# Performance work log

Measured on AMD Instinct MI355X. Metric: run time of the kernel, lower is better.

## Reference

```python
import jax, jax.numpy as jnp
import numpy as np

INPUT_DIM, ENC_H, DEC_H, HORIZON = 8, 384, 384, 18
B, L = 1024, 336


def _lstm_layer(xs, Wih, Whh, bih, bhh):
    # xs: [B, L, D] -> outputs [B, L, H], final h [B, H]
    Bv = xs.shape[0]
    Hh = Whh.shape[1]
    def step(carry, x_t):
        h, c = carry
        z = x_t @ Wih.T + h @ Whh.T + bih + bhh  # [B, 4H], gate order i,f,g,o (PyTorch)
        i, f, g, o = jnp.split(z, 4, axis=-1)
        c = jax.nn.sigmoid(f) * c + jax.nn.sigmoid(i) * jnp.tanh(g)
        h = jax.nn.sigmoid(o) * jnp.tanh(c)
        return (h, c), h
    init = (jnp.zeros((Bv, Hh), xs.dtype), jnp.zeros((Bv, Hh), xs.dtype))
    (h, c), ys = jax.lax.scan(step, init, jnp.swapaxes(xs, 0, 1))
    return jnp.swapaxes(ys, 0, 1), h


def setup_inputs() -> dict:
    key = jax.random.key(0)
    ks = jax.random.split(key, 20)
    s = 0.05
    d = {
        "x": jax.random.normal(ks[0], (B, L, INPUT_DIM), jnp.float32),
        "future_feats": jax.random.normal(ks[1], (B, HORIZON, 4), jnp.float32),
        # encoder layer 0
        "enc_Wih0": jax.random.normal(ks[2], (4 * ENC_H, INPUT_DIM), jnp.float32) * s,
        "enc_Whh0": jax.random.normal(ks[3], (4 * ENC_H, ENC_H), jnp.float32) * s,
        "enc_bih0": jax.random.normal(ks[4], (4 * ENC_H,), jnp.float32) * s,
        "enc_bhh0": jax.random.normal(ks[5], (4 * ENC_H,), jnp.float32) * s,
        # encoder layer 1
        "enc_Wih1": jax.random.normal(ks[6], (4 * ENC_H, ENC_H), jnp.float32) * s,
        "enc_Whh1": jax.random.normal(ks[7], (4 * ENC_H, ENC_H), jnp.float32) * s,
        "enc_bih1": jax.random.normal(ks[8], (4 * ENC_H,), jnp.float32) * s,
        "enc_bhh1": jax.random.normal(ks[9], (4 * ENC_H,), jnp.float32) * s,
        # attention projection (no bias)
        "Wa": jax.random.normal(ks[10], (DEC_H, ENC_H), jnp.float32) * s,
        # dec_in: Linear(1+4+enc_h -> dec_h)
        "dec_in_W": jax.random.normal(ks[11], (DEC_H, 1 + 4 + ENC_H), jnp.float32) * s,
        "dec_in_b": jax.random.normal(ks[12], (DEC_H,), jnp.float32) * s,
        # decoder LSTM (1 layer)
        "dec_Wih": jax.random.normal(ks[13], (4 * DEC_H, DEC_H), jnp.float32) * s,
        "dec_Whh": jax.random.normal(ks[14], (4 * DEC_H, DEC_H), jnp.float32) * s,
        "dec_bih": jax.random.normal(ks[15], (4 * DEC_H,), jnp.float32) * s,
        "dec_bhh": jax.random.normal(ks[16], (4 * DEC_H,), jnp.float32) * s,
        # output head
        "out_W": jax.random.normal(ks[17], (1, DEC_H), jnp.float32) * s,
        "out_b": jax.random.normal(ks[18], (1,), jnp.float32) * s,
    }
    return d


def reference(x, future_feats, enc_Wih0, enc_Whh0, enc_bih0, enc_bhh0,
              enc_Wih1, enc_Whh1, enc_bih1, enc_bhh1, Wa, dec_in_W, dec_in_b,
              dec_Wih, dec_Whh, dec_bih, dec_bhh, out_W, out_b):
    Bv = x.shape[0]
    # 2-layer encoder (eval mode: inter-layer dropout inactive)
    h1, _ = _lstm_layer(x, enc_Wih0, enc_Whh0, enc_bih0, enc_bhh0)
    enc_out, h_last = _lstm_layer(h1, enc_Wih1, enc_Whh1, enc_bih1, enc_bhh1)
    proj = enc_out @ Wa.T  # [B, L, dec_h] (Wa(enc_out) is step-invariant)

    def dec_step(carry, feat_t):
        h, c, y_prev = carry
        scores = jnp.einsum('bld,bd->bl', proj, h)
        alpha = jax.nn.softmax(scores, axis=1)
        ctx = jnp.einsum('bl,bld->bd', alpha, enc_out)
        din = jnp.concatenate([y_prev, feat_t, ctx], axis=1)  # [B, 1+4+enc_h]
        din = jax.nn.relu(din @ dec_in_W.T + dec_in_b)
        z = din @ dec_Wih.T + h @ dec_Whh.T + dec_bih + dec_bhh
        i, f, g, o = jnp.split(z, 4, axis=-1)
        c = jax.nn.sigmoid(f) * c + jax.nn.sigmoid(i) * jnp.tanh(g)
        h = jax.nn.sigmoid(o) * jnp.tanh(c)
        y_t = h @ out_W.T + out_b  # [B, 1]
        y_prev = jax.lax.stop_gradient(y_t)  # .detach() in torch
        return (h, c, y_prev), y_t

    init = (h_last, jnp.zeros_like(h_last), jnp.zeros((Bv, 1), x.dtype))
    _, ys = jax.lax.scan(dec_step, init, jnp.swapaxes(future_feats, 0, 1))
    return jnp.swapaxes(ys, 0, 1)  # [B, horizon, 1]
```

## Files before the change

### kernel.cpp

```cpp
#include <hip/hip_runtime.h>
#include <stdint.h>

typedef __bf16 bf16;
typedef __bf16 bf16x8 __attribute__((ext_vector_type(8)));
typedef short  s16x8  __attribute__((ext_vector_type(8)));
typedef float  f32x4  __attribute__((ext_vector_type(4)));
typedef uint32_t u32;

#define NB   1024
#define LSEQ 336
#define HID  384
#define HOR  18
#define SMEM_BYTES 36864
#define E1T  ((size_t)24*NB*16)

__device__ bf16  g_H0[(size_t)(LSEQ+1)*NB*HID];
__device__ bf16  g_E1[(size_t)(LSEQ+1)*E1T];
__device__ bf16  g_enc[(size_t)NB*LSEQ*HID];
__device__ bf16  g_Adec[2*NB*768];
__device__ bf16  g_Adin[NB*416];
__device__ bf16  g_xb[NB*LSEQ*8];
__device__ float g_cdec[NB*HID];
__device__ float g_u[NB*HID];
__device__ float g_bias0[1536], g_bias1[1536], g_biasd[1536], g_biasdin[384];
__device__ bf16  g_Bp0[12*13*4096];
__device__ bf16  g_Bp1n[24*24*4*64*8];
__device__ bf16  g_Bpd[12*24*4096];
__device__ bf16  g_Bpi[3*13*4096];
__device__ bf16  g_Bpu[3*12*4096];
__device__ int   g_f0 [8*LSEQ*12*16];
__device__ int   g_f0m[8*LSEQ*12*16];
__device__ int   g_f1 [4*(LSEQ+1)*24*16];

__device__ __forceinline__ float sigf(float x){ return 1.0f/(1.0f + __expf(-x)); }
__device__ __forceinline__ float tanh_f(float x){
  x = fminf(fmaxf(x, -15.f), 15.f);
  float e = __expf(2.f*x);
  return (e - 1.f)/(e + 1.f);
}

__global__ void zero_state_k(){
  int i = blockIdx.x*blockDim.x + threadIdx.x;
  int st = gridDim.x*blockDim.x;
  bf16 z = (bf16)0.f;
  for(int k=i;k<NB*HID;k+=st){ g_H0[k]=z; g_E1[k]=z; g_cdec[k]=0.f; }
  for(int k=i;k<8*LSEQ*12*16;k+=st){ g_f0[k]=0; g_f0m[k]=0; }
  for(int k=i;k<4*(LSEQ+1)*24*16;k+=st) g_f1[k]=0;
}

__global__ void pack_xb_k(const float* __restrict__ x){
  int i = blockIdx.x*256 + threadIdx.x;
  int n = NB*LSEQ*8;
  for(int k=i; k<n; k+=gridDim.x*256) g_xb[k] = (bf16)x[k];
}

__global__ void pack_gates_k(int mode, const float* __restrict__ W1, const float* __restrict__ W2,
                             int nks){
  bf16* out = (mode==0)? g_Bp0 : g_Bpd;
  size_t idx = (size_t)blockIdx.x*256 + threadIdx.x;
  size_t total = (size_t)12*nks*512;
  if(idx >= total) return;
  int lane = (int)(idx & 63);
  int tt   = (int)((idx>>6) & 7);
  size_t tmp = idx >> 9;
  int ks = (int)(tmp % nks);
  int jb = (int)(tmp / nks);
  int n  = (tt>>1)*HID + jb*32 + (tt&1)*16 + (lane&15);
  int kb = ks*32 + (lane>>4)*8;
  bf16x8 v;
  #pragma unroll
  for(int i=0;i<8;i++){
    int k = kb + i;
    float f;
    if(mode==0) f = (k<384) ? W1[(size_t)n*384 + k] : (k<392 ? W2[(size_t)n*8 + (k-384)] : 0.f);
    else        f = (k<384) ? W1[(size_t)n*384 + k] : W2[(size_t)n*384 + (k-384)];
    v[i] = (bf16)f;
  }
  *(bf16x8*)(out + idx*8) = v;
}

__global__ void pack_gates16_k(const float* __restrict__ Wih1, const float* __restrict__ Whh1){
  int idx = blockIdx.x*256 + threadIdx.x;
  if(idx >= 24*24*4*64) return;
  int lane = idx&63, rem = idx>>6;
  int g = rem&3; rem >>= 2;
  int ks = rem%24, jn = rem/24;
  int n  = g*HID + jn*16 + (lane&15);
  int kb = ks*32 + (lane>>4)*8;
  bf16x8 v;
  #pragma unroll
  for(int i=0;i<8;i++){
    int k = kb+i;
    float f = (k<384)? Wih1[(size_t)n*384 + k] : Whh1[(size_t)n*384 + (k-384)];
    v[i] = (bf16)f;
  }
  *(bf16x8*)(g_Bp1n + (size_t)idx*8) = v;
}

__global__ void pack_plain_k(int mode, const float* __restrict__ W, int nks, int nb_cnt){
  bf16* out = mode ? g_Bpu : g_Bpi;
  size_t idx = (size_t)blockIdx.x*256 + threadIdx.x;
  size_t total = (size_t)nb_cnt*nks*512;
  if(idx>=total) return;
  int lane = (int)(idx&63);
  int tt   = (int)((idx>>6)&7);
  size_t tmp = idx>>9;
  int ks = (int)(tmp%nks);
  int nb = (int)(tmp/nks);
  int n  = nb*128 + tt*16 + (lane&15);
  int kb = ks*32 + (lane>>4)*8;
  bf16x8 v;
  #pragma unroll
  for(int i=0;i<8;i++){
    int k = kb+i;
    float f;
    if(mode==0) f = (k<389)? W[(size_t)n*389 + k] : 0.f;
    else        f = W[(size_t)k*384 + n];
    v[i]=(bf16)f;
  }
  *(bf16x8*)(out + idx*8) = v;
}

__global__ void prep_misc_k(const float* bih0,const float* bhh0,const float* bih1,const float* bhh1,
                            const float* dbih,const float* dbhh,const float* dinb){
  int i = blockIdx.x*256 + threadIdx.x;
  if(i<1536){ g_bias0[i]=bih0[i]+bhh0[i]; g_bias1[i]=bih1[i]+bhh1[i]; g_biasd[i]=dbih[i]+dbhh[i]; }
  if(i<384) g_biasdin[i]=dinb[i];
}

__device__ __forceinline__ void spin_set(int* p){
  while(__hip_atomic_load(p, __ATOMIC_RELAXED, __HIP_MEMORY_SCOPE_AGENT) == 0)
    __builtin_amdgcn_s_sleep(2);
}
__device__ __forceinline__ void flag_set(int* p){
  __hip_atomic_store(p, 1, __ATOMIC_RELAXED, __HIP_MEMORY_SCOPE_AGENT);
}
__device__ __forceinline__ void release_agent(){
  __builtin_amdgcn_fence(__ATOMIC_RELEASE, "agent");
}

__global__ __launch_bounds__(256,1)
void enc10_k(){
  extern __shared__ char lds[];
  const int bid = blockIdx.x, tid = threadIdx.x;
  const int lane = tid&63, wv = tid>>6;
  const int l15 = lane&15, lk = (lane>>4)*8;

  if(bid < 96){
    const int g = bid & 7, jb = bid >> 3;
    { const s16x8* src = (const s16x8*)(g_Bp0 + (size_t)jb*13*4096);
      s16x8* dst = (s16x8*)lds;
      #pragma unroll
      for(int h=0;h<26;h++) dst[tid + h*256] = src[tid + h*256];
    }
    bf16* tr = (bf16*)(lds + 13*8192);
    __syncthreads();
    const int jj0 = jb*32 + l15;
    float bia[2],bfa[2],bga[2],boa[2];
    #pragma unroll
    for(int jh=0;jh<2;jh++){
      bia[jh]=g_bias0[jj0+jh*16];     bfa[jh]=g_bias0[384+jj0+jh*16];
      bga[jh]=g_bias0[768+jj0+jh*16]; boa[jh]=g_bias0[1152+jj0+jh*16];
    }
    size_t hoff[2], xoff[2];
    #pragma unroll
    for(int mt=0;mt<2;mt++){
      int row = g*128 + wv*32 + mt*16 + l15;
      hoff[mt] = (size_t)row*HID + lk;
      xoff[mt] = (size_t)row*LSEQ*8;
    }
    float c[2][2][4] = {};
    for(int w=0; w<LSEQ; w++){
      if(w>=1 && tid<12) spin_set(&g_f0[((g*LSEQ + (w-1))*12 + tid)*16]);
      __syncthreads();
      asm volatile("" ::: "memory");
      const bf16* H0w = g_H0 + (size_t)w*NB*HID;
      bf16x8 af[13][2];
      #pragma unroll
      for(int ks=0;ks<12;ks++)
        #pragma unroll
        for(int mt=0;mt<2;mt++)
          af[ks][mt] = *(const bf16x8*)(H0w + hoff[mt] + ks*32);
      #pragma unroll
      for(int mt=0;mt<2;mt++){
        bf16x8 z;
        #pragma unroll
        for(int e=0;e<8;e++) z[e]=(bf16)0.f;
        if(lk==0) z = *(const bf16x8*)(g_xb + xoff[mt] + (size_t)w*8);
        af[12][mt] = z;
      }
      f32x4 acc[2][8];
      #pragma unroll
      for(int m2=0;m2<2;m2++)
        #pragma unroll
        for(int tt=0;tt<8;tt++) acc[m2][tt] = (f32x4){0.f,0.f,0.f,0.f};
      #pragma unroll
      for(int ks=0;ks<13;ks++){
        #pragma unroll
        for(int tt=0;tt<8;tt++){
          bf16x8 bfr = *(const bf16x8*)(lds + (ks*8+tt)*1024 + lane*16);
          acc[0][tt] = __builtin_amdgcn_mfma_f32_16x16x32_bf16(af[ks][0], bfr, acc[0][tt],0,0,0);
          acc[1][tt] = __builtin_amdgcn_mfma_f32_16x16x32_bf16(af[ks][1], bfr, acc[1][tt],0,0,0);
        }
      }
      #pragma unroll
      for(int mt=0;mt<2;mt++)
        #pragma unroll
        for(int jh=0;jh<2;jh++)
          #pragma unroll
          for(int r=0;r<4;r++){
            float zi=acc[mt][0+jh][r]+bia[jh], zf=acc[mt][2+jh][r]+bfa[jh],
                  zg=acc[mt][4+jh][r]+bga[jh], zo=acc[mt][6+jh][r]+boa[jh];
            float cn = sigf(zf)*c[mt][jh][r] + sigf(zi)*tanh_f(zg);
            c[mt][jh][r]=cn;
            int lr = wv*32 + mt*16 + (lane>>4)*4 + r;
            tr[lr*32 + jh*16 + l15] = (bf16)(sigf(zo)*tanh_f(cn));
          }
      __syncthreads();
      bf16* H0n = g_H0 + (size_t)(w+1)*NB*HID;
      #pragma unroll
      for(int h=0;h<2;h++){
        int p = tid + h*256;
        int row = p>>2, cc = p&3;
        s16x8 v = *(const s16x8*)(tr + row*32 + cc*8);
        *(s16x8*)(H0n + (size_t)(g*128+row)*HID + jb*32 + cc*8) = v;
      }
      __syncthreads();
      if(tid==0){
        release_agent();
        flag_set(&g_f0 [((g*LSEQ + w)*12 + jb)*16]);
        flag_set(&g_f0m[((g*LSEQ + w)*12 + jb)*16]);
      }
    }
  } else {
    const int idx = bid-96, m = (idx&7)>>1, jn = (idx>>3) + (idx&1)*12;
    { const s16x8* src = (const s16x8*)(g_Bp1n + (size_t)jn*24*2048);
      s16x8* dst = (s16x8*)lds;
      #pragma unroll
      for(int h=0;h<24;h++) dst[tid + h*256] = src[tid + h*256];
    }
    bf16* tr = (bf16*)(lds + 24*4096);
    __syncthreads();
    const int jj = jn*16 + l15;
    const float bi=g_bias1[jj], bff=g_bias1[384+jj], bg=g_bias1[768+jj], bo=g_bias1[1152+jj];
    int rows[4]; size_t hoff[4], eo[4];
    const int jn_half = (lane>>4)>>1, colin = ((lane>>4)&1)*8;
    #pragma unroll
    for(int mt=0;mt<4;mt++){
      rows[mt] = m*256 + wv*64 + mt*16 + l15;
      hoff[mt] = (size_t)rows[mt]*HID + lk;
      eo[mt]   = (size_t)jn_half*(NB*16) + (size_t)rows[mt]*16 + colin;
    }
    float c[4][4] = {};
    for(int s=1; s<=LSEQ; s++){
      if(tid<24){
        int gg = 2*m + (tid>=12);
        spin_set(&g_f0m[((gg*LSEQ + (s-1))*12 + (tid%12))*16]);
      }
      __syncthreads();
      asm volatile("" ::: "memory");
      const bf16* H0s = g_H0 + (size_t)s*NB*HID;
      const bf16* Es  = g_E1 + (size_t)(s-1)*E1T;
      bf16x8 ap[8][4];
      #pragma unroll
      for(int d=0; d<8; d++)
        #pragma unroll
        for(int mt=0;mt<4;mt++)
          ap[d][mt] = *(const bf16x8*)(H0s + hoff[mt] + d*32);
      if(s>=2 && tid>=32 && tid<56)
        spin_set(&g_f1[((m*(LSEQ+1) + (s-1))*24 + (tid-32))*16]);
      __syncthreads();
      asm volatile("" ::: "memory");
      f32x4 acc[4][4];
      #pragma unroll
      for(int mt=0;mt<4;mt++)
        #pragma unroll
        for(int g4=0;g4<4;g4++) acc[mt][g4] = (f32x4){0.f,0.f,0.f,0.f};
      #pragma unroll
      for(int ks=0;ks<24;ks++){
        bf16x8 bfr[4];
        #pragma unroll
        for(int g4=0;g4<4;g4++) bfr[g4] = *(const bf16x8*)(lds + (ks*4+g4)*1024 + lane*16);
        bf16x8 a[4];
        #pragma unroll
        for(int mt=0;mt<4;mt++) a[mt] = ap[ks&7][mt];
        int kn = ks+8;
        if(kn<24){
          if(kn<12){
            #pragma unroll
            for(int mt=0;mt<4;mt++) ap[ks&7][mt] = *(const bf16x8*)(H0s + hoff[mt] + kn*32);
          } else {
            #pragma unroll
            for(int mt=0;mt<4;mt++) ap[ks&7][mt] = *(const bf16x8*)(Es + (size_t)(kn-12)*32768 + eo[mt]);
          }
        }
        #pragma unroll
        for(int mt=0;mt<4;mt++)
          #pragma unroll
          for(int g4=0;g4<4;g4++)
            acc[mt][g4] = __builtin_amdgcn_mfma_f32_16x16x32_bf16(a[mt], bfr[g4], acc[mt][g4],0,0,0);
      }
      #pragma unroll
      for(int mt=0;mt<4;mt++)
        #pragma unroll
        for(int r=0;r<4;r++){
          float zi=acc[mt][0][r]+bi, zf=acc[mt][1][r]+bff,
                zg=acc[mt][2][r]+bg, zo=acc[mt][3][r]+bo;
          float cn = sigf(zf)*c[mt][r] + sigf(zi)*tanh_f(zg);
          c[mt][r]=cn;
          int lr = wv*64 + mt*16 + (lane>>4)*4 + r;
          tr[lr*16 + l15] = (bf16)(sigf(zo)*tanh_f(cn));
        }
      __syncthreads();
      bf16* E1w = g_E1 + (size_t)s*E1T + (size_t)jn*(NB*16);
      #pragma unroll
      for(int h=0;h<2;h++){
        int p = tid + h*256;
        int row = p>>1, hf2 = p&1;
        s16x8 v = *(const s16x8*)(tr + row*16 + hf2*8);
        *(s16x8*)(E1w + (size_t)(m*256+row)*16 + hf2*8) = v;
      }
      __syncthreads();
      if(tid==0){
        release_agent();
        flag_set(&g_f1[((m*(LSEQ+1) + s)*24 + jn)*16]);
      }
      if((jn&1)==0 && s>=2){
        const int t_out = s-2;
        const bf16* Ep = g_E1 + (size_t)(s-1)*E1T;
        #pragma unroll
        for(int h=0;h<4;h++){
          int cch = tid + h*256;
          int row = cch>>2, seg = cch&3;
          const bf16* srcp = Ep + (size_t)(jn + (seg>>1))*(NB*16) + (size_t)(m*256+row)*16 + (seg&1)*8;
          s16x8 v = *(const s16x8*)srcp;
          *(s16x8*)(g_enc + ((size_t)(m*256+row)*LSEQ + t_out)*HID + jn*16 + seg*8) = v;
        }
      }
    }
    if(tid<24) spin_set(&g_f1[((m*(LSEQ+1) + LSEQ)*24 + tid)*16]);
    __syncthreads();
    asm volatile("" ::: "memory");
    if((jn&1)==0){
      const bf16* Ep = g_E1 + (size_t)LSEQ*E1T;
      #pragma unroll
      for(int h=0;h<4;h++){
        int cch = tid + h*256;
        int row = cch>>2, seg = cch&3;
        const bf16* srcp = Ep + (size_t)(jn + (seg>>1))*(NB*16) + (size_t)(m*256+row)*16 + (seg&1)*8;
        s16x8 v = *(const s16x8*)srcp;
        *(s16x8*)(g_enc + ((size_t)(m*256+row)*LSEQ + (LSEQ-1))*HID + jn*16 + seg*8) = v;
      }
    }
  }
}

struct SReg { s16x8 a0,a1,b0,b1; };

__device__ __forceinline__ void stage_load(const bf16* __restrict__ A, int ldA,
                                           const bf16* __restrict__ Bk, int tid, SReg& sr){
  int c0 = tid, c1 = tid+256;
  sr.a0 = *(const s16x8*)(A + (size_t)(c0>>2)*ldA + (c0&3)*8);
  sr.a1 = *(const s16x8*)(A + (size_t)(c1>>2)*ldA + (c1&3)*8);
  const s16x8* B8 = (const s16x8*)Bk;
  sr.b0 = B8[c0]; sr.b1 = B8[c1];
}

__device__ __forceinline__ void stage_write(char* Ab, char* Bb, int tid, const SReg& sr){
  int c0 = tid, c1 = tid+256;
  *(s16x8*)(Ab + (c0>>2)*80 + (c0&3)*16) = sr.a0;
  *(s16x8*)(Ab + (c1>>2)*80 + (c1&3)*16) = sr.a1;
  *(s16x8*)(Bb + c0*16) = sr.b0;
  *(s16x8*)(Bb + c1*16) = sr.b1;
}

__device__ __forceinline__ void gemm_core(const bf16* __restrict__ A, int ldA,
                                          const bf16* __restrict__ Bp, int nks,
                                          char* smem, f32x4 acc[4][4]){
  const int tid = threadIdx.x;
  const int lane = tid & 63, wv = tid>>6, wm = wv>>1, wn = wv&1;
  char* Ab0 = smem;            char* Ab1 = smem + 10240;
  char* Bb0 = smem + 20480;    char* Bb1 = smem + 28672;
  f32x4 z = {0.f,0.f,0.f,0.f};
  #pragma unroll
  for(int m=0;m<4;m++)
    #pragma unroll
    for(int g=0;g<4;g++) acc[m][g]=z;
  SReg sr;
  stage_load(A, ldA, Bp, tid, sr);
  stage_write(Ab0, Bb0, tid, sr);
  const int aoff = (wm*64 + (lane&15))*80 + (lane>>4)*16;
  const int boff = wn*1024 + lane*16;
  for(int ks=0; ks<nks; ks++){
    char* Ac = (ks&1)? Ab1: Ab0;
    char* Bc = (ks&1)? Bb1: Bb0;
    char* An = (ks&1)? Ab0: Ab1;
    char* Bn = (ks&1)? Bb0: Bb1;
    bool more = (ks+1)<nks;
    if(more) stage_load(A + (ks+1)*32, ldA, Bp + (size_t)(ks+1)*4096, tid, sr);
    __syncthreads();
    bf16x8 af[4], bfr[4];
    #pragma unroll
    for(int mt=0;mt<4;mt++) af[mt] = *(const bf16x8*)(Ac + aoff + mt*16*80);
    #pragma unroll
    for(int g=0;g<4;g++)    bfr[g] = *(const bf16x8*)(Bc + boff + g*2048);
    #pragma unroll
    for(int mt=0;mt<4;mt++)
      #pragma unroll
      for(int g=0;g<4;g++)
        acc[mt][g] = __builtin_amdgcn_mfma_f32_16x16x32_bf16(af[mt], bfr[g], acc[mt][g], 0,0,0);
    if(more) stage_write(An, Bn, tid, sr);
  }
}

__device__ __forceinline__ void lstm_epi(f32x4 acc[4][4], int mbase, int jb,
     const float* __restrict__ bias, float* __restrict__ cst,
     bf16* __restrict__ d0, int ld0, bf16* __restrict__ d1, size_t ld1){
  int lane = threadIdx.x&63, wv = threadIdx.x>>6, wm = wv>>1, wn = wv&1;
  int j = jb*32 + wn*16 + (lane&15);
  float bi = bias[j], bff = bias[384+j], bg = bias[768+j], bo = bias[1152+j];
  #pragma unroll
  for(int mt=0;mt<4;mt++){
    #pragma unroll
    for(int r=0;r<4;r++){
      int brow = mbase + wm*64 + mt*16 + (lane>>4)*4 + r;
      float zi = acc[mt][0][r]+bi, zf = acc[mt][1][r]+bff,
            zg = acc[mt][2][r]+bg, zo = acc[mt][3][r]+bo;
      size_t ci = (size_t)brow*HID + j;
      float cold = cst[ci];
      float cn = sigf(zf)*cold + sigf(zi)*tanh_f(zg);
      cst[ci] = cn;
      bf16 hb = (bf16)(sigf(zo)*tanh_f(cn));
      d0[(size_t)brow*ld0 + j] = hb;
      if(d1) d1[(size_t)brow*ld1 + j] = hb;
    }
  }
}

__global__ __launch_bounds__(256)
void dec_lstm_k(int t){
  __shared__ char smem[SMEM_BYTES];
  int bid = blockIdx.x, mb = bid/12, jb = bid%12;
  int rs = t&1, wsl = rs^1;
  f32x4 acc[4][4];
  gemm_core(g_Adec + (size_t)rs*NB*768 + (size_t)mb*128*768, 768,
            g_Bpd + (size_t)jb*24*4096, 24, smem, acc);
  lstm_epi(acc, mb*128, jb, g_biasd, g_cdec,
           g_Adec + (size_t)wsl*NB*768 + 384, 768, (bf16*)nullptr, 0);
}

__global__ __launch_bounds__(256)
void plain_gemm_k(int t, int mode, const float* __restrict__ outW,
                  const float* __restrict__ outb, float* __restrict__ out,
                  const float* __restrict__ ff){
  __shared__ char smem[SMEM_BYTES];
  int bid = blockIdx.x, mb = bid/3, nb = bid%3;
  int rs = t&1;
  const bf16* A; int ldA, nks; const bf16* Bp;
  if(mode==1){ A = g_Adec + (size_t)rs*NB*768 + 384; ldA=768; Bp = g_Bpu; nks=12; }
  else       { A = g_Adin;                           ldA=416; Bp = g_Bpi; nks=13; }
  f32x4 acc[4][4];
  gemm_core(A + (size_t)mb*128*ldA, ldA, Bp + (size_t)nb*nks*4096, nks, smem, acc);
  int lane = threadIdx.x&63, wv = threadIdx.x>>6, wm = wv>>1, wn = wv&1;
  bf16* dbf = g_Adec + (size_t)rs*NB*768;
  #pragma unroll
  for(int mt=0;mt<4;mt++){
    #pragma unroll
    for(int ti=0;ti<4;ti++){
      int n = nb*128 + (ti*2+wn)*16 + (lane&15);
      #pragma unroll
      for(int r=0;r<4;r++){
        int brow = mb*128 + wm*64 + mt*16 + (lane>>4)*4 + r;
        float v = acc[mt][ti][r];
        if(mode==0){ v += g_biasdin[n]; v = fmaxf(v,0.f); dbf[(size_t)brow*768 + n] = (bf16)v; }
        else g_u[(size_t)brow*384 + n] = v;
      }
    }
  }
  if(mode==1 && t>=1 && nb==0 && threadIdx.x<128){
    int b = mb*128 + threadIdx.x;
    const s16x8* hp = (const s16x8*)(g_Adec + (size_t)rs*NB*768 + (size_t)b*768 + 384);
    float acc2 = 0.f;
    #pragma unroll 4
    for(int i=0;i<48;i++){
      s16x8 v = hp[i];
      #pragma unroll
      for(int e=0;e<8;e++){
        float hv = __uint_as_float(((u32)(uint16_t)v[e])<<16);
        acc2 += hv*outW[i*8+e];
      }
    }
    float y = acc2 + outb[0];
    out[(size_t)b*HOR + (t-1)] = y;
    g_Adin[(size_t)b*416] = (bf16)y;
    #pragma unroll
    for(int k=0;k<4;k++) g_Adin[(size_t)b*416 + 1 + k] = (bf16)ff[(size_t)b*HOR*4 + t*4 + k];
  }
}

__global__ __launch_bounds__(256)
void attn_k(int t){
  __shared__ float sm[4][392];
  int tid = threadIdx.x, lane = tid&63, w = tid>>6;
  int bl = w>>1, hf = w&1;
  int b = blockIdx.x*2 + bl;
  const float* ub = g_u + (size_t)b*HID + lane*6;
  float u0=ub[0],u1=ub[1],u2=ub[2],u3=ub[3],u4=ub[4],u5=ub[5];
  const u32* er = (const u32*)(g_enc + (size_t)b*LSEQ*HID) + (size_t)hf*168*192 + lane*3;
  int estep = 192;
  if(t & 1){ er += (size_t)167*192; estep = -192; }
  float m=-1e30f, den=0.f, a0=0,a1=0,a2=0,a3=0,a4=0,a5=0;
  for(int l=0;l<168;l++){
    u32 w0 = er[0], w1 = er[1], w2 = er[2];
    er += estep;
    float e0 = __uint_as_float(w0<<16);
    float e1 = __uint_as_float(w0 & 0xffff0000u);
    float e2 = __uint_as_float(w1<<16);
    float e3 = __uint_as_float(w1 & 0xffff0000u);
    float e4 = __uint_as_float(w2<<16);
    float e5 = __uint_as_float(w2 & 0xffff0000u);
    float p = e0*u0 + e1*u1 + e2*u2 + e3*u3 + e4*u4 + e5*u5;
    #pragma unroll
    for(int o=1;o<64;o<<=1) p += __shfl_xor(p, o, 64);
    float mn = fmaxf(m, p);
    float al = __expf(m - mn), pe = __expf(p - mn);
    den = den*al + pe;
    a0 = a0*al + pe*e0; a1 = a1*al + pe*e1; a2 = a2*al + pe*e2;
    a3 = a3*al + pe*e3; a4 = a4*al + pe*e4; a5 = a5*al + pe*e5;
    m = mn;
  }
  if(lane==0){ sm[w][0]=m; sm[w][1]=den; }
  sm[w][2+lane*6+0]=a0; sm[w][2+lane*6+1]=a1; sm[w][2+lane*6+2]=a2;
  sm[w][2+lane*6+3]=a3; sm[w][2+lane*6+4]=a4; sm[w][2+lane*6+5]=a5;
  __syncthreads();
  if(hf==0){
    float m2 = sm[w+1][0], d2 = sm[w+1][1];
    float M = fmaxf(m, m2);
    float f1 = __expf(m - M), f2 = __expf(m2 - M);
    float inv = 1.f/(den*f1 + d2*f2);
    bf16* cd = g_Adin + (size_t)b*416 + 5 + lane*6;
    cd[0] = (bf16)((a0*f1 + sm[w+1][2+lane*6+0]*f2)*inv);
    cd[1] = (bf16)((a1*f1 + sm[w+1][2+lane*6+1]*f2)*inv);
    cd[2] = (bf16)((a2*f1 + sm[w+1][2+lane*6+2]*f2)*inv);
    cd[3] = (bf16)((a3*f1 + sm[w+1][2+lane*6+3]*f2)*inv);
    cd[4] = (bf16)((a4*f1 + sm[w+1][2+lane*6+4]*f2)*inv);
    cd[5] = (bf16)((a5*f1 + sm[w+1][2+lane*6+5]*f2)*inv);
  }
}

__global__ void post_k(int t, const float* __restrict__ outW,
                       const float* __restrict__ outb, float* __restrict__ out){
  int b = blockIdx.x*256 + threadIdx.x;
  if(b>=NB) return;
  int wsl = (t&1)^1;
  const s16x8* hp = (const s16x8*)(g_Adec + (size_t)wsl*NB*768 + (size_t)b*768 + 384);
  float acc = 0.f;
  #pragma unroll 4
  for(int i=0;i<48;i++){
    s16x8 v = hp[i];
    #pragma unroll
    for(int e=0;e<8;e++){
      float hv = __uint_as_float(((u32)(uint16_t)v[e])<<16);
      acc += hv*outW[i*8+e];
    }
  }
  out[(size_t)b*HOR + t] = acc + outb[0];
}

__global__ void dec_prep_k(const float* __restrict__ ff){
  int i = blockIdx.x*256 + threadIdx.x;
  if(i < NB*HID){
    int b = i/HID, j = i%HID;
    g_Adec[(size_t)b*768 + 384 + j] = g_enc[(size_t)b*LSEQ*HID + (size_t)(LSEQ-1)*HID + j];
  }
  if(i < NB*4){
    int b = i>>2, k = i&3;
    g_Adin[(size_t)b*416 + 1 + k] = (bf16)ff[(size_t)b*HOR*4 + k];
  }
  if(i < NB) g_Adin[(size_t)i*416] = (bf16)0.f;
}

extern "C" void kernel_launch(void* const* d_in, const int* in_sizes, int n_in,
                              void* d_out, int out_size, void* d_ws, size_t ws_size,
                              hipStream_t stream){
  const float* x    = (const float*)d_in[0];
  const float* ff   = (const float*)d_in[1];
  const float* Wih0 = (const float*)d_in[2];
  const float* Whh0 = (const float*)d_in[3];
  const float* bih0 = (const float*)d_in[4];
  const float* bhh0 = (const float*)d_in[5];
  const float* Wih1 = (const float*)d_in[6];
  const float* Whh1 = (const float*)d_in[7];
  const float* bih1 = (const float*)d_in[8];
  const float* bhh1 = (const float*)d_in[9];
  const float* Wa   = (const float*)d_in[10];
  const float* dinW = (const float*)d_in[11];
  const float* dinb = (const float*)d_in[12];
  const float* dWih = (const float*)d_in[13];
  const float* dWhh = (const float*)d_in[14];
  const float* dbih = (const float*)d_in[15];
  const float* dbhh = (const float*)d_in[16];
  const float* outW = (const float*)d_in[17];
  const float* outb = (const float*)d_in[18];
  float* out = (float*)d_out;

  zero_state_k<<<1024,256,0,stream>>>();
  pack_xb_k<<<2048,256,0,stream>>>(x);
  pack_gates_k<<<(12*13*512)/256,256,0,stream>>>(0, Whh0, Wih0, 13);
  pack_gates16_k<<<576,256,0,stream>>>(Wih1, Whh1);
  pack_gates_k<<<(12*24*512)/256,256,0,stream>>>(2, dWih, dWhh, 24);
  pack_plain_k<<<(3*13*512)/256,256,0,stream>>>(0, dinW, 13, 3);
  pack_plain_k<<<(3*12*512)/256,256,0,stream>>>(1, Wa, 12, 3);
  prep_misc_k<<<8,256,0,stream>>>(bih0,bhh0,bih1,bhh1,dbih,dbhh,dinb);

  hipFuncSetAttribute((const void*)enc10_k,
                      hipFuncAttributeMaxDynamicSharedMemorySize, 114688);
  enc10_k<<<192,256,114688,stream>>>();

  dec_prep_k<<<1536,256,0,stream>>>(ff);
  for(int t=0;t<HOR;t++){
    plain_gemm_k<<<24,256,0,stream>>>(t, 1, outW, outb, out, ff);
    attn_k<<<512,256,0,stream>>>(t);
    plain_gemm_k<<<24,256,0,stream>>>(t, 0, outW, outb, out, ff);
    dec_lstm_k<<<96,256,0,stream>>>(t);
  }
  post_k<<<4,256,0,stream>>>(17, outW, outb, out);
  (void)in_sizes; (void)n_in; (void)out_size; (void)d_ws; (void)ws_size;
}
```

Measured before the change: 7.595 ms.

## Fuse attention query projection and output head into attention kernel

Removes the per-step MFMA GEMM that computed u = h·Wa into a global buffer. Each attention block now computes its two rows of u itself from a bf16 copy of Wa using scalar FMAs in LDS, and the y_t output dot product moves into otherwise idle threads of the same block. This drops one kernel launch per decoder step and the global round trip of u. The cost is that Wa is read redundantly by all 512 blocks and the projection runs on plain FMAs instead of matrix cores. Encoder output stores also become nontemporal, and the unused second destination is dropped from the LSTM epilogue.

```diff
diff --git a/kernel.cpp b/kernel.cpp
--- a/kernel.cpp
+++ b/kernel.cpp
@@ -20,14 +20,13 @@
 __device__ bf16  g_Adec[2*NB*768];
 __device__ bf16  g_Adin[NB*416];
 __device__ bf16  g_xb[NB*LSEQ*8];
+__device__ bf16  g_Wab[HID*HID];
 __device__ float g_cdec[NB*HID];
-__device__ float g_u[NB*HID];
 __device__ float g_bias0[1536], g_bias1[1536], g_biasd[1536], g_biasdin[384];
 __device__ bf16  g_Bp0[12*13*4096];
 __device__ bf16  g_Bp1n[24*24*4*64*8];
 __device__ bf16  g_Bpd[12*24*4096];
 __device__ bf16  g_Bpi[3*13*4096];
-__device__ bf16  g_Bpu[3*12*4096];
 __device__ int   g_f0 [8*LSEQ*12*16];
 __device__ int   g_f0m[8*LSEQ*12*16];
 __device__ int   g_f1 [4*(LSEQ+1)*24*16];
@@ -48,10 +47,11 @@
   for(int k=i;k<4*(LSEQ+1)*24*16;k+=st) g_f1[k]=0;
 }
 
-__global__ void pack_xb_k(const float* __restrict__ x){
+__global__ void pack_xb_k(const float* __restrict__ x, const float* __restrict__ Wa){
   int i = blockIdx.x*256 + threadIdx.x;
   int n = NB*LSEQ*8;
   for(int k=i; k<n; k+=gridDim.x*256) g_xb[k] = (bf16)x[k];
+  for(int k=i; k<HID*HID; k+=gridDim.x*256) g_Wab[k] = (bf16)Wa[k];
 }
 
 __global__ void pack_gates_k(int mode, const float* __restrict__ W1, const float* __restrict__ W2,
@@ -97,8 +97,8 @@
   *(bf16x8*)(g_Bp1n + (size_t)idx*8) = v;
 }
 
-__global__ void pack_plain_k(int mode, const float* __restrict__ W, int nks, int nb_cnt){
-  bf16* out = mode ? g_Bpu : g_Bpi;
+__global__ void pack_plain_k(const float* __restrict__ W, int nks, int nb_cnt){
+  bf16* out = g_Bpi;
   size_t idx = (size_t)blockIdx.x*256 + threadIdx.x;
   size_t total = (size_t)nb_cnt*nks*512;
   if(idx>=total) return;
@@ -113,9 +113,7 @@
   #pragma unroll
   for(int i=0;i<8;i++){
     int k = kb+i;
-    float f;
-    if(mode==0) f = (k<389)? W[(size_t)n*389 + k] : 0.f;
-    else        f = W[(size_t)k*384 + n];
+    float f = (k<389)? W[(size_t)n*389 + k] : 0.f;
     v[i]=(bf16)f;
   }
   *(bf16x8*)(out + idx*8) = v;
@@ -140,7 +138,7 @@
 }
 
 __global__ __launch_bounds__(256,1)
-void enc10_k(){
+void enc11_k(){
   extern __shared__ char lds[];
   const int bid = blockIdx.x, tid = threadIdx.x;
   const int lane = tid&63, wv = tid>>6;
@@ -334,7 +332,7 @@
           int row = cch>>2, seg = cch&3;
           const bf16* srcp = Ep + (size_t)(jn + (seg>>1))*(NB*16) + (size_t)(m*256+row)*16 + (seg&1)*8;
           s16x8 v = *(const s16x8*)srcp;
-          *(s16x8*)(g_enc + ((size_t)(m*256+row)*LSEQ + t_out)*HID + jn*16 + seg*8) = v;
+          __builtin_nontemporal_store(v, (s16x8*)(g_enc + ((size_t)(m*256+row)*LSEQ + t_out)*HID + jn*16 + seg*8));
         }
       }
     }
@@ -349,7 +347,7 @@
         int row = cch>>2, seg = cch&3;
         const bf16* srcp = Ep + (size_t)(jn + (seg>>1))*(NB*16) + (size_t)(m*256+row)*16 + (seg&1)*8;
         s16x8 v = *(const s16x8*)srcp;
-        *(s16x8*)(g_enc + ((size_t)(m*256+row)*LSEQ + (LSEQ-1))*HID + jn*16 + seg*8) = v;
+        __builtin_nontemporal_store(v, (s16x8*)(g_enc + ((size_t)(m*256+row)*LSEQ + (LSEQ-1))*HID + jn*16 + seg*8));
       }
     }
   }
@@ -415,7 +413,7 @@
 
 __device__ __forceinline__ void lstm_epi(f32x4 acc[4][4], int mbase, int jb,
      const float* __restrict__ bias, float* __restrict__ cst,
-     bf16* __restrict__ d0, int ld0, bf16* __restrict__ d1, size_t ld1){
+     bf16* __restrict__ d0, int ld0){
   int lane = threadIdx.x&63, wv = threadIdx.x>>6, wm = wv>>1, wn = wv&1;
   int j = jb*32 + wn*16 + (lane&15);
   float bi = bias[j], bff = bias[384+j], bg = bias[768+j], bo = bias[1152+j];
@@ -430,9 +428,7 @@
       float cold = cst[ci];
       float cn = sigf(zf)*cold + sigf(zi)*tanh_f(zg);
       cst[ci] = cn;
-      bf16 hb = (bf16)(sigf(zo)*tanh_f(cn));
-      d0[(size_t)brow*ld0 + j] = hb;
-      if(d1) d1[(size_t)brow*ld1 + j] = hb;
+      d0[(size_t)brow*ld0 + j] = (bf16)(sigf(zo)*tanh_f(cn));
     }
   }
 }
@@ -446,21 +442,16 @@
   gemm_core(g_Adec + (size_t)rs*NB*768 + (size_t)mb*128*768, 768,
             g_Bpd + (size_t)jb*24*4096, 24, smem, acc);
   lstm_epi(acc, mb*128, jb, g_biasd, g_cdec,
-           g_Adec + (size_t)wsl*NB*768 + 384, 768, (bf16*)nullptr, 0);
+           g_Adec + (size_t)wsl*NB*768 + 384, 768);
 }
 
 __global__ __launch_bounds__(256)
-void plain_gemm_k(int t, int mode, const float* __restrict__ outW,
-                  const float* __restrict__ outb, float* __restrict__ out,
-                  const float* __restrict__ ff){
+void din_gemm_k(int t){
   __shared__ char smem[SMEM_BYTES];
   int bid = blockIdx.x, mb = bid/3, nb = bid%3;
   int rs = t&1;
-  const bf16* A; int ldA, nks; const bf16* Bp;
-  if(mode==1){ A = g_Adec + (size_t)rs*NB*768 + 384; ldA=768; Bp = g_Bpu; nks=12; }
-  else       { A = g_Adin;                           ldA=416; Bp = g_Bpi; nks=13; }
   f32x4 acc[4][4];
-  gemm_core(A + (size_t)mb*128*ldA, ldA, Bp + (size_t)nb*nks*4096, nks, smem, acc);
+  gemm_core(g_Adin + (size_t)mb*128*416, 416, g_Bpi + (size_t)nb*13*4096, 13, smem, acc);
   int lane = threadIdx.x&63, wv = threadIdx.x>>6, wm = wv>>1, wn = wv&1;
   bf16* dbf = g_Adec + (size_t)rs*NB*768;
   #pragma unroll
@@ -471,40 +462,65 @@
       #pragma unroll
       for(int r=0;r<4;r++){
         int brow = mb*128 + wm*64 + mt*16 + (lane>>4)*4 + r;
-        float v = acc[mt][ti][r];
-        if(mode==0){ v += g_biasdin[n]; v = fmaxf(v,0.f); dbf[(size_t)brow*768 + n] = (bf16)v; }
-        else g_u[(size_t)brow*384 + n] = v;
-      }
-    }
-  }
-  if(mode==1 && t>=1 && nb==0 && threadIdx.x<128){
-    int b = mb*128 + threadIdx.x;
-    const s16x8* hp = (const s16x8*)(g_Adec + (size_t)rs*NB*768 + (size_t)b*768 + 384);
-    float acc2 = 0.f;
-    #pragma unroll 4
-    for(int i=0;i<48;i++){
-      s16x8 v = hp[i];
-      #pragma unroll
-      for(int e=0;e<8;e++){
-        float hv = __uint_as_float(((u32)(uint16_t)v[e])<<16);
-        acc2 += hv*outW[i*8+e];
-      }
-    }
-    float y = acc2 + outb[0];
-    out[(size_t)b*HOR + (t-1)] = y;
-    g_Adin[(size_t)b*416] = (bf16)y;
-    #pragma unroll
-    for(int k=0;k<4;k++) g_Adin[(size_t)b*416 + 1 + k] = (bf16)ff[(size_t)b*HOR*4 + t*4 + k];
+        float v = acc[mt][ti][r] + g_biasdin[n];
+        v = fmaxf(v,0.f);
+        dbf[(size_t)brow*768 + n] = (bf16)v;
+      }
+    }
   }
 }
 
 __global__ __launch_bounds__(256)
-void attn_k(int t){
+void attn_k(int t, const float* __restrict__ outW, const float* __restrict__ outb,
+            float* __restrict__ out, const float* __restrict__ ff){
   __shared__ float sm[4][392];
+  __shared__ float us[2][384];
+  __shared__ float hs[2][384];
   int tid = threadIdx.x, lane = tid&63, w = tid>>6;
   int bl = w>>1, hf = w&1;
-  int b = blockIdx.x*2 + bl;
-  const float* ub = g_u + (size_t)b*HID + lane*6;
+  int b0 = blockIdx.x*2;
+  int rs = t&1;
+  for(int i=tid; i<768; i+=256){
+    int r = i>>8 ? (i>=384) : 0;
+    r = (i>=384);
+    int e = i - r*384;
+    hs[r][e] = (float)g_Adec[(size_t)rs*NB*768 + (size_t)(b0+r)*768 + 384 + e];
+  }
+  __syncthreads();
+  if(tid < 192){
+    float a00=0.f,a01=0.f,a10=0.f,a11=0.f;
+    const u32* wp = (const u32*)g_Wab + tid;
+    #pragma unroll 4
+    for(int d=0; d<384; d++){
+      u32 wvv = wp[(size_t)d*192];
+      float w0 = __uint_as_float(wvv<<16);
+      float w1 = __uint_as_float(wvv & 0xffff0000u);
+      float h0 = hs[0][d], h1 = hs[1][d];
+      a00 += h0*w0; a01 += h0*w1;
+      a10 += h1*w0; a11 += h1*w1;
+    }
+    us[0][2*tid]=a00; us[0][2*tid+1]=a01;
+    us[1][2*tid]=a10; us[1][2*tid+1]=a11;
+  } else if(t >= 1){
+    int l = tid - 192;
+    int r = l>>5, j0 = (l&31)*12;
+    float acc2 = 0.f;
+    #pragma unroll
+    for(int i2=0;i2<12;i2++) acc2 += hs[r][j0+i2]*outW[j0+i2];
+    #pragma unroll
+    for(int o=1;o<32;o<<=1) acc2 += __shfl_xor(acc2, o, 64);
+    if((l&31)==0){
+      int b = b0 + r;
+      float y = acc2 + outb[0];
+      out[(size_t)b*HOR + (t-1)] = y;
+      g_Adin[(size_t)b*416] = (bf16)y;
+      #pragma unroll
+      for(int k=0;k<4;k++) g_Adin[(size_t)b*416 + 1 + k] = (bf16)ff[(size_t)b*HOR*4 + t*4 + k];
+    }
+  }
+  __syncthreads();
+  int b = b0 + bl;
+  const float* ub = us[bl] + lane*6;
   float u0=ub[0],u1=ub[1],u2=ub[2],u3=ub[3],u4=ub[4],u5=ub[5];
   const u32* er = (const u32*)(g_enc + (size_t)b*LSEQ*HID) + (size_t)hf*168*192 + lane*3;
   int estep = 192;
@@ -605,23 +621,21 @@
   float* out = (float*)d_out;
 
   zero_state_k<<<1024,256,0,stream>>>();
-  pack_xb_k<<<2048,256,0,stream>>>(x);
+  pack_xb_k<<<2048,256,0,stream>>>(x, Wa);
   pack_gates_k<<<(12*13*512)/256,256,0,stream>>>(0, Whh0, Wih0, 13);
   pack_gates16_k<<<576,256,0,stream>>>(Wih1, Whh1);
   pack_gates_k<<<(12*24*512)/256,256,0,stream>>>(2, dWih, dWhh, 24);
-  pack_plain_k<<<(3*13*512)/256,256,0,stream>>>(0, dinW, 13, 3);
-  pack_plain_k<<<(3*12*512)/256,256,0,stream>>>(1, Wa, 12, 3);
+  pack_plain_k<<<(3*13*512)/256,256,0,stream>>>(dinW, 13, 3);
   prep_misc_k<<<8,256,0,stream>>>(bih0,bhh0,bih1,bhh1,dbih,dbhh,dinb);
 
-  hipFuncSetAttribute((const void*)enc10_k,
+  hipFuncSetAttribute((const void*)enc11_k,
                       hipFuncAttributeMaxDynamicSharedMemorySize, 114688);
-  enc10_k<<<192,256,114688,stream>>>();
+  enc11_k<<<192,256,114688,stream>>>();
 
   dec_prep_k<<<1536,256,0,stream>>>(ff);
   for(int t=0;t<HOR;t++){
-    plain_gemm_k<<<24,256,0,stream>>>(t, 1, outW, outb, out, ff);
-    attn_k<<<512,256,0,stream>>>(t);
-    plain_gemm_k<<<24,256,0,stream>>>(t, 0, outW, outb, out, ff);
+    attn_k<<<512,256,0,stream>>>(t, outW, outb, out, ff);
+    din_gemm_k<<<24,256,0,stream>>>(t);
     dec_lstm_k<<<96,256,0,stream>>>(t);
   }
   post_k<<<4,256,0,stream>>>(17, outW, outb, out);
```

New measurement: 7.621 ms. About the same (+0.3%).
